# Kernel tuning notes

Measured on AMD Instinct MI355X. Metric: run time of the kernel, lower is better.

## Reference

```python
import jax, jax.numpy as jnp
import numpy as np

H = 16           # num_heads
D = 1024         # hidden_size
HD = D // H      # head_dim = 64
LN_EPS = 1e-5


def setup_inputs() -> dict:
    key = jax.random.key(0)
    ks = jax.random.split(key, 11)
    s = 1.0 / np.sqrt(D)
    x = jax.random.normal(ks[0], (2, 2048, D), dtype=jnp.float32)
    Wq = jax.random.uniform(ks[1], (D, D), jnp.float32, -s, s)
    bq = jax.random.uniform(ks[2], (D,), jnp.float32, -s, s)
    Wk = jax.random.uniform(ks[3], (D, D), jnp.float32, -s, s)
    bk = jax.random.uniform(ks[4], (D,), jnp.float32, -s, s)
    Wv = jax.random.uniform(ks[5], (D, D), jnp.float32, -s, s)
    bv = jax.random.uniform(ks[6], (D,), jnp.float32, -s, s)
    Wo = jax.random.uniform(ks[7], (D, D), jnp.float32, -s, s)
    bo = jax.random.uniform(ks[8], (D,), jnp.float32, -s, s)
    gamma = jnp.ones((D,), jnp.float32)
    beta = jnp.zeros((D,), jnp.float32)
    return {"x": x, "Wq": Wq, "bq": bq, "Wk": Wk, "bk": bk,
            "Wv": Wv, "bv": bv, "Wo": Wo, "bo": bo,
            "gamma": gamma, "beta": beta}


def reference(x, Wq, bq, Wk, bk, Wv, bv, Wo, bo, gamma, beta):
    B, S, _ = x.shape
    # projections -> [B, H, S, HD]
    def split_heads(t):
        return t.reshape(B, S, H, HD).transpose(0, 2, 1, 3)
    Q = split_heads(x @ Wq + bq)
    K = split_heads(x @ Wk + bk)
    V = split_heads(x @ Wv + bv)
    # scores [B, H, S, S], softmax over keys (dropout = identity in eval)
    scores = jnp.einsum('bhqd,bhkd->bhqk', Q, K) / np.sqrt(HD).astype(np.float32)
    attn = jax.nn.softmax(scores, axis=-1)
    ctx = jnp.einsum('bhqk,bhkd->bhqd', attn, V)          # [B, H, S, HD]
    ctx = ctx.transpose(0, 2, 1, 3).reshape(B, S, H * HD)  # [B, S, D]
    out = ctx @ Wo + bo
    # residual + LayerNorm
    y = out + x
    mu = jnp.mean(y, axis=-1, keepdims=True)
    var = jnp.mean(jnp.square(y - mu), axis=-1, keepdims=True)
    return (y - mu) * jax.lax.rsqrt(var + LN_EPS) * gamma + beta
```

## Files before the change

### kernel.cpp

```cpp
#include <hip/hip_runtime.h>
#include <cstdint>
#include <cstddef>


typedef short  b16x8  __attribute__((ext_vector_type(8)));
typedef float  f32x4  __attribute__((ext_vector_type(4)));
typedef float  f32x16 __attribute__((ext_vector_type(16)));

#define AS1 __attribute__((address_space(1)))
#define AS3 __attribute__((address_space(3)))

__device__ __forceinline__ unsigned short f2bf(float f) {
    unsigned int u = __builtin_bit_cast(unsigned int, f);
    u += 0x7FFFu + ((u >> 16) & 1u);
    return (unsigned short)(u >> 16);
}

__device__ __forceinline__ unsigned int cvt_pk_bf16(float lo, float hi) {
    unsigned int r;
    asm("v_cvt_pk_bf16_f32 %0, %1, %2" : "=v"(r) : "v"(lo), "v"(hi));
    return r;
}

__device__ __forceinline__ float exp2_fast(float x) {
    float r;
    asm("v_exp_f32 %0, %1" : "=v"(r) : "v"(x));
    return r;
}

__device__ __forceinline__ void permswap(unsigned &a, unsigned &b) {
    asm volatile("v_permlane32_swap_b32 %0, %1" : "+v"(a), "+v"(b));
}

__global__ __launch_bounds__(256) void k_cvt_x(const float* __restrict__ x,
                                               unsigned short* __restrict__ xb) {
    int i = blockIdx.x * 256 + threadIdx.x;
    float4 v = ((const float4*)x)[i];
    ushort4 o;
    o.x = f2bf(v.x); o.y = f2bf(v.y); o.z = f2bf(v.z); o.w = f2bf(v.w);
    ((ushort4*)xb)[i] = o;
}

__global__ __launch_bounds__(1024) void k_cvt_w(
    const float* __restrict__ W0, const float* __restrict__ W1,
    const float* __restrict__ W2, const float* __restrict__ W3,
    unsigned short* __restrict__ T0, unsigned short* __restrict__ T1,
    unsigned short* __restrict__ T2, unsigned short* __restrict__ T3) {
    const float* W = blockIdx.z == 0 ? W0 : blockIdx.z == 1 ? W1 : blockIdx.z == 2 ? W2 : W3;
    unsigned short* T = blockIdx.z == 0 ? T0 : blockIdx.z == 1 ? T1 : blockIdx.z == 2 ? T2 : T3;
    __shared__ float tile[32][33];
    int k0 = blockIdx.x * 32, n0 = blockIdx.y * 32;
    int tx = threadIdx.x, ty = threadIdx.y;
    tile[ty][tx] = W[(size_t)(k0 + ty) * 1024 + n0 + tx];
    __syncthreads();
    T[(size_t)(n0 + ty) * 1024 + k0 + tx] = f2bf(tile[tx][ty]);
}

__global__ __launch_bounds__(512) void k_gemm_qkv(
    const unsigned short* __restrict__ A, const unsigned short* __restrict__ Bt,
    const float* __restrict__ bq, const float* __restrict__ bk, const float* __restrict__ bv,
    unsigned short* __restrict__ Qb, unsigned short* __restrict__ Kt,
    unsigned short* __restrict__ Vt) {
    __shared__ unsigned short As[2][256 * 32];
    __shared__ unsigned short Bs[2][96 * 32];
    const int tid = threadIdx.x, lane = tid & 63, wid = tid >> 6;
    const int m0 = blockIdx.y * 256, n0 = blockIdx.x * 96;
    const int wr = wid >> 1, wc = wid & 1;
    f32x4 acc[4][3] = {};

    const int srow = tid >> 2, scol = (tid & 3) * 8;
    const unsigned short* Ag  = A  + (size_t)(m0 + srow) * 1024 + scol;
    const unsigned short* Ag2 = A  + (size_t)(m0 + 128 + srow) * 1024 + scol;
    const unsigned short* Bg  = Bt + (size_t)(n0 + srow) * 1024 + scol;

#define GSTAGE(kt, buf) do {                                                              \
        __builtin_amdgcn_global_load_lds((const AS1 void*)(Ag  + (kt) * 32),              \
                                         (AS3 void*)((char*)As[buf] + tid * 16),        16, 0, 0); \
        __builtin_amdgcn_global_load_lds((const AS1 void*)(Ag2 + (kt) * 32),              \
                                         (AS3 void*)((char*)As[buf] + 8192 + tid * 16), 16, 0, 0); \
        if (tid < 384)                                                                    \
            __builtin_amdgcn_global_load_lds((const AS1 void*)(Bg + (kt) * 32),           \
                                             (AS3 void*)((char*)Bs[buf] + tid * 16),    16, 0, 0); \
    } while (0)

    GSTAGE(0, 0);
    __syncthreads();

    const int g = lane >> 4, r = lane & 15;
    for (int kt = 0; kt < 32; ++kt) {
        const int cur = kt & 1;
        if (kt < 31) GSTAGE(kt + 1, cur ^ 1);
        b16x8 af[4], bfr[3];
#pragma unroll
        for (int mi = 0; mi < 4; ++mi)
            af[mi] = __builtin_bit_cast(b16x8, *(const uint4*)(As[cur] + (wr * 64 + mi * 16 + r) * 32 + g * 8));
#pragma unroll
        for (int ni = 0; ni < 3; ++ni)
            bfr[ni] = __builtin_bit_cast(b16x8, *(const uint4*)(Bs[cur] + (wc * 48 + ni * 16 + r) * 32 + g * 8));
#pragma unroll
        for (int mi = 0; mi < 4; ++mi)
#pragma unroll
            for (int ni = 0; ni < 3; ++ni)
                acc[mi][ni] = __builtin_amdgcn_mfma_f32_16x16x32_bf16(af[mi], bfr[ni], acc[mi][ni], 0, 0, 0);
        __syncthreads();
    }
#undef GSTAGE

    for (int ni = 0; ni < 3; ++ni) {
        int col = n0 + wc * 48 + ni * 16 + r;
        int which = col >> 10, c = col & 1023;
        const float* bp = which == 0 ? bq : which == 1 ? bk : bv;
        float bvv = bp[c];
        int h = c >> 6, hd = c & 63;
        for (int mi = 0; mi < 4; ++mi)
            for (int j = 0; j < 4; ++j) {
                int row = m0 + wr * 64 + mi * 16 + g * 4 + j;
                float v = acc[mi][ni][j] + bvv;
                int b = row >> 11, s = row & 2047;
                size_t bh = (size_t)(b * 16 + h);
                if (which == 0) {
                    Qb[(bh * 2048 + s) * 64 + hd] = f2bf(v * 0.180336881f);
                } else if (which == 1) {
                    int tt = s >> 6, kr = s & 63;
                    Kt[(bh * 32 + tt) * 4096 + ((kr * 64 + hd) ^ ((kr & 7) << 3))] = f2bf(v);
                } else {
                    int tt = s >> 6, cc = s & 63;
                    Vt[(bh * 32 + tt) * 4096 + ((hd * 64 + cc) ^ ((hd & 7) << 3))] = f2bf(v);
                }
            }
    }
}

__global__ __launch_bounds__(512) void k_gemm_proj(
    const unsigned short* __restrict__ A, const unsigned short* __restrict__ Bt,
    const float* __restrict__ bias, float* __restrict__ out) {
    __shared__ unsigned short As[2][128 * 32];
    __shared__ unsigned short Bs[2][64 * 32];
    const int tid = threadIdx.x, lane = tid & 63, wid = tid >> 6;
    const int m0 = blockIdx.y * 128, n0 = blockIdx.x * 64;
    const int wr = wid >> 1, wc = wid & 1;
    f32x4 acc[2][2] = {};

    const int srow = tid >> 2, scol = (tid & 3) * 8;
    const unsigned short* Ag = A  + (size_t)(m0 + srow) * 1024 + scol;
    const unsigned short* Bg = Bt + (size_t)(n0 + srow) * 1024 + scol;

#define PSTAGE(kt, buf) do {                                                              \
        __builtin_amdgcn_global_load_lds((const AS1 void*)(Ag + (kt) * 32),               \
                                         (AS3 void*)((char*)As[buf] + tid * 16), 16, 0, 0); \
        if (tid < 256)                                                                    \
            __builtin_amdgcn_global_load_lds((const AS1 void*)(Bg + (kt) * 32),           \
                                             (AS3 void*)((char*)Bs[buf] + tid * 16), 16, 0, 0); \
    } while (0)

    PSTAGE(0, 0);
    __syncthreads();

    const int g = lane >> 4, r = lane & 15;
    for (int kt = 0; kt < 32; ++kt) {
        const int cur = kt & 1;
        if (kt < 31) PSTAGE(kt + 1, cur ^ 1);
        b16x8 af[2], bfr[2];
#pragma unroll
        for (int mi = 0; mi < 2; ++mi)
            af[mi] = __builtin_bit_cast(b16x8, *(const uint4*)(As[cur] + (wr * 32 + mi * 16 + r) * 32 + g * 8));
#pragma unroll
        for (int ni = 0; ni < 2; ++ni)
            bfr[ni] = __builtin_bit_cast(b16x8, *(const uint4*)(Bs[cur] + (wc * 32 + ni * 16 + r) * 32 + g * 8));
#pragma unroll
        for (int mi = 0; mi < 2; ++mi)
#pragma unroll
            for (int ni = 0; ni < 2; ++ni)
                acc[mi][ni] = __builtin_amdgcn_mfma_f32_16x16x32_bf16(af[mi], bfr[ni], acc[mi][ni], 0, 0, 0);
        __syncthreads();
    }
#undef PSTAGE

    for (int mi = 0; mi < 2; ++mi)
        for (int ni = 0; ni < 2; ++ni) {
            int col = n0 + wc * 32 + ni * 16 + r;
            float bv = bias[col];
            for (int j = 0; j < 4; ++j) {
                int row = m0 + wr * 32 + mi * 16 + g * 4 + j;
                out[(size_t)row * 1024 + col] = acc[mi][ni][j] + bv;
            }
        }
}

#define TSWZ(row, byteoff) ((((row) * 128) + (byteoff)) ^ (((row) & 7) << 4))

__global__ __launch_bounds__(256, 2) void k_attn(const unsigned short* __restrict__ Qb,
                                                 const unsigned short* __restrict__ Kt,
                                                 const unsigned short* __restrict__ Vt,
                                                 unsigned short* __restrict__ ctx) {
    __shared__ unsigned short Ks[2][4096];
    __shared__ unsigned short Vs[2][4096];
    const int tid = threadIdx.x, lane = tid & 63, w = tid >> 6;
    const int q32 = lane & 31, hi = lane >> 5;

    int bid = blockIdx.x;
    int xcd = bid & 7, idx = bid >> 3;
    int bh = xcd * 4 + (idx & 3);
    int q0 = (idx >> 2) * 128;
    const int b = bh >> 4, h = bh & 15;

    const unsigned short* qrow = Qb + ((size_t)bh * 2048 + q0 + w * 32 + q32) * 64 + hi * 8;
    b16x8 qf[4];
#pragma unroll
    for (int ds = 0; ds < 4; ++ds)
        qf[ds] = __builtin_bit_cast(b16x8, *(const uint4*)(qrow + ds * 16));

    const unsigned short* Kg = Kt + (size_t)bh * 32 * 4096;
    const unsigned short* Vg = Vt + (size_t)bh * 32 * 4096;

#define STAGE(kt, buf) do {                                                               \
        const unsigned short* _ks = Kg + (size_t)(kt) * 4096 + tid * 8;                   \
        const unsigned short* _vs = Vg + (size_t)(kt) * 4096 + tid * 8;                   \
        __builtin_amdgcn_global_load_lds((const AS1 void*)_ks,          (AS3 void*)((char*)Ks[buf] + tid * 16),        16, 0, 0); \
        __builtin_amdgcn_global_load_lds((const AS1 void*)(_ks + 2048), (AS3 void*)((char*)Ks[buf] + 4096 + tid * 16), 16, 0, 0); \
        __builtin_amdgcn_global_load_lds((const AS1 void*)_vs,          (AS3 void*)((char*)Vs[buf] + tid * 16),        16, 0, 0); \
        __builtin_amdgcn_global_load_lds((const AS1 void*)(_vs + 2048), (AS3 void*)((char*)Vs[buf] + 4096 + tid * 16), 16, 0, 0); \
    } while (0)

    float m_run = -1e30f, lpart = 0.f;
    f32x16 oacc[2] = {};

    STAGE(0, 0);
    __syncthreads();

    for (int kt = 0; kt < 32; ++kt) {
        const int cur = kt & 1;
        if (kt < 31) STAGE(kt + 1, cur ^ 1);

        f32x16 sacc[2] = {};
#pragma unroll
        for (int ds = 0; ds < 4; ++ds) {
            b16x8 kf0 = __builtin_bit_cast(b16x8, *(const uint4*)((char*)Ks[cur] + TSWZ(q32,      ds * 32 + hi * 16)));
            b16x8 kf1 = __builtin_bit_cast(b16x8, *(const uint4*)((char*)Ks[cur] + TSWZ(32 + q32, ds * 32 + hi * 16)));
            sacc[0] = __builtin_amdgcn_mfma_f32_32x32x16_bf16(kf0, qf[ds], sacc[0], 0, 0, 0);
            sacc[1] = __builtin_amdgcn_mfma_f32_32x32x16_bf16(kf1, qf[ds], sacc[1], 0, 0, 0);
        }

        float m8[8];
#pragma unroll
        for (int i = 0; i < 8; ++i)
            m8[i] = fmaxf(fmaxf(sacc[0][i], sacc[0][i + 8]), fmaxf(sacc[1][i], sacc[1][i + 8]));
        float mx = fmaxf(fmaxf(fmaxf(m8[0], m8[1]), fmaxf(m8[2], m8[3])),
                         fmaxf(fmaxf(m8[4], m8[5]), fmaxf(m8[6], m8[7])));
        {
            unsigned a = __builtin_bit_cast(unsigned, mx), bb = a;
            permswap(a, bb);
            mx = fmaxf(__builtin_bit_cast(float, a), __builtin_bit_cast(float, bb));
        }
        if (!__all(mx <= m_run + 8.f)) {
            float mn = fmaxf(m_run, mx);
            float al = exp2_fast(m_run - mn);
            m_run = mn;
            lpart *= al;
#pragma unroll
            for (int reg = 0; reg < 16; ++reg) {
                int qr = (reg & 3) + 8 * (reg >> 2) + 4 * hi;
                float ar = __shfl(al, qr, 64);
                oacc[0][reg] *= ar;
                oacc[1][reg] *= ar;
            }
        }
        float pb[2][16];
#pragma unroll
        for (int kb = 0; kb < 2; ++kb)
#pragma unroll
            for (int reg = 0; reg < 16; ++reg) {
                float p = exp2_fast(sacc[kb][reg] - m_run);
                pb[kb][reg] = p;
                lpart += p;
            }
        unsigned wv[2][4][2];
#pragma unroll
        for (int kb = 0; kb < 2; ++kb)
#pragma unroll
            for (int rg = 0; rg < 4; ++rg) {
                wv[kb][rg][0] = cvt_pk_bf16(pb[kb][rg * 4 + 0], pb[kb][rg * 4 + 1]);
                wv[kb][rg][1] = cvt_pk_bf16(pb[kb][rg * 4 + 2], pb[kb][rg * 4 + 3]);
            }
        b16x8 pa[4];
#pragma unroll
        for (int ks = 0; ks < 4; ++ks) {
            int kb = ks >> 1, rg0 = (ks & 1) * 2;
            unsigned u0 = wv[kb][rg0][0], u2 = wv[kb][rg0 + 1][0];
            permswap(u0, u2);
            unsigned u1 = wv[kb][rg0][1], u3 = wv[kb][rg0 + 1][1];
            permswap(u1, u3);
            uint4 uu; uu.x = u0; uu.y = u1; uu.z = u2; uu.w = u3;
            pa[ks] = __builtin_bit_cast(b16x8, uu);
        }
#pragma unroll
        for (int ks = 0; ks < 4; ++ks) {
            b16x8 vf0 = __builtin_bit_cast(b16x8, *(const uint4*)((char*)Vs[cur] + TSWZ(q32,      ks * 32 + hi * 16)));
            b16x8 vf1 = __builtin_bit_cast(b16x8, *(const uint4*)((char*)Vs[cur] + TSWZ(32 + q32, ks * 32 + hi * 16)));
            oacc[0] = __builtin_amdgcn_mfma_f32_32x32x16_bf16(pa[ks], vf0, oacc[0], 0, 0, 0);
            oacc[1] = __builtin_amdgcn_mfma_f32_32x32x16_bf16(pa[ks], vf1, oacc[1], 0, 0, 0);
        }
        __syncthreads();
    }

    {
        unsigned a = __builtin_bit_cast(unsigned, lpart), bb = a;
        permswap(a, bb);
        lpart = __builtin_bit_cast(float, a) + __builtin_bit_cast(float, bb);
    }
    float invl = 1.f / lpart;
#pragma unroll
    for (int reg = 0; reg < 16; ++reg) {
        int qr = (reg & 3) + 8 * (reg >> 2) + 4 * hi;
        float iv = __shfl(invl, qr, 64);
        unsigned short* dst = ctx + ((size_t)(b * 2048 + q0 + w * 32 + qr)) * 1024 + h * 64 + q32;
        dst[0]  = f2bf(oacc[0][reg] * iv);
        dst[32] = f2bf(oacc[1][reg] * iv);
    }
#undef STAGE
}

__global__ __launch_bounds__(256) void k_ln(const float* __restrict__ proj,
                                            const float* __restrict__ x,
                                            const float* __restrict__ gamma,
                                            const float* __restrict__ beta,
                                            float* __restrict__ out) {
    int t = threadIdx.x, lane = t & 63, w = t >> 6;
    int row = blockIdx.x * 4 + w;
    const float4* pr = (const float4*)(proj + (size_t)row * 1024);
    const float4* xr = (const float4*)(x    + (size_t)row * 1024);
    float4 y[4];
    float s = 0.f, ss = 0.f;
#pragma unroll
    for (int i = 0; i < 4; ++i) {
        float4 a = pr[lane + i * 64], bx = xr[lane + i * 64];
        float4 yy;
        yy.x = a.x + bx.x; yy.y = a.y + bx.y; yy.z = a.z + bx.z; yy.w = a.w + bx.w;
        y[i] = yy;
        s  += yy.x + yy.y + yy.z + yy.w;
        ss += yy.x * yy.x + yy.y * yy.y + yy.z * yy.z + yy.w * yy.w;
    }
#pragma unroll
    for (int o = 32; o > 0; o >>= 1) {
        s  += __shfl_xor(s,  o, 64);
        ss += __shfl_xor(ss, o, 64);
    }
    float mu  = s * (1.f / 1024.f);
    float var = ss * (1.f / 1024.f) - mu * mu;
    float inv = rsqrtf(var + 1e-5f);
    float4* outr = (float4*)(out + (size_t)row * 1024);
    const float4* gr = (const float4*)gamma;
    const float4* br = (const float4*)beta;
#pragma unroll
    for (int i = 0; i < 4; ++i) {
        float4 g4 = gr[lane + i * 64], b4 = br[lane + i * 64];
        float4 o4;
        o4.x = (y[i].x - mu) * inv * g4.x + b4.x;
        o4.y = (y[i].y - mu) * inv * g4.y + b4.y;
        o4.z = (y[i].z - mu) * inv * g4.z + b4.z;
        o4.w = (y[i].w - mu) * inv * g4.w + b4.w;
        outr[lane + i * 64] = o4;
    }
}

extern "C" void kernel_launch(void* const* d_in, const int* in_sizes, int n_in,
                              void* d_out, int out_size, void* d_ws, size_t ws_size,
                              hipStream_t stream) {
    const float* x  = (const float*)d_in[0];
    const float* Wq = (const float*)d_in[1];
    const float* bq = (const float*)d_in[2];
    const float* Wk = (const float*)d_in[3];
    const float* bk = (const float*)d_in[4];
    const float* Wv = (const float*)d_in[5];
    const float* bv = (const float*)d_in[6];
    const float* Wo = (const float*)d_in[7];
    const float* bo = (const float*)d_in[8];
    const float* gamma = (const float*)d_in[9];
    const float* beta  = (const float*)d_in[10];

    char* ws = (char*)d_ws;
    const size_t MB = 1u << 20;
    unsigned short* xbf   = (unsigned short*)(ws);
    unsigned short* Wqkvt = (unsigned short*)(ws + 8 * MB);
    unsigned short* Wot   = (unsigned short*)(ws + 14 * MB);
    unsigned short* Qb    = (unsigned short*)(ws + 16 * MB);
    unsigned short* Kt    = (unsigned short*)(ws + 24 * MB);
    unsigned short* Vt    = (unsigned short*)(ws + 32 * MB);
    float* proj = (float*)(ws + 16 * MB);
    unsigned short* ctx = xbf;

    k_cvt_x<<<4096, 256, 0, stream>>>(x, xbf);
    k_cvt_w<<<dim3(32, 32, 4), dim3(32, 32), 0, stream>>>(
        Wq, Wk, Wv, Wo, Wqkvt, Wqkvt + 1024 * 1024, Wqkvt + 2 * 1024 * 1024, Wot);
    k_gemm_qkv<<<dim3(32, 16), 512, 0, stream>>>(xbf, Wqkvt, bq, bk, bv, Qb, Kt, Vt);
    k_attn<<<512, 256, 0, stream>>>(Qb, Kt, Vt, ctx);
    k_gemm_proj<<<dim3(16, 32), 512, 0, stream>>>(ctx, Wot, bo, proj);
    k_ln<<<1024, 256, 0, stream>>>(proj, x, gamma, beta, (float*)d_out);
}
```

Before: 141.3 us.

## Split attention KV range across two warp groups and merge partial softmax results

The attention kernel now launches 512 threads per block. Two groups of four waves each process half of the 32 key tiles for the same 128 queries, each group with its own double-buffered K/V LDS region. At the end, group 1 writes its partial output accumulators and (max, sum) into reused LDS, and group 0 combines them with a log-sum-exp rescale before writing ctx. This split-K scheme adds parallelism per block to hide latency, at the cost of doubled LDS use, an extra merge step, and lower register budget per thread under the new launch bounds.

```diff
diff --git a/kernel.cpp b/kernel.cpp
--- a/kernel.cpp
+++ b/kernel.cpp
@@ -189,14 +189,17 @@
 
 #define TSWZ(row, byteoff) ((((row) * 128) + (byteoff)) ^ (((row) & 7) << 4))
 
-__global__ __launch_bounds__(256, 2) void k_attn(const unsigned short* __restrict__ Qb,
+__global__ __launch_bounds__(512, 4) void k_attn(const unsigned short* __restrict__ Qb,
                                                  const unsigned short* __restrict__ Kt,
                                                  const unsigned short* __restrict__ Vt,
                                                  unsigned short* __restrict__ ctx) {
-    __shared__ unsigned short Ks[2][4096];
-    __shared__ unsigned short Vs[2][4096];
+    __shared__ unsigned short Ks[2][2][4096];
+    __shared__ unsigned short Vs[2][2][4096];
+    __shared__ float2 ml[4][64];
     const int tid = threadIdx.x, lane = tid & 63, w = tid >> 6;
     const int q32 = lane & 31, hi = lane >> 5;
+    const int wq = w & 3, grp = w >> 2;
+    const int lt = wq * 64 + lane;
 
     int bid = blockIdx.x;
     int xcd = bid & 7, idx = bid >> 3;
@@ -204,7 +207,7 @@
     int q0 = (idx >> 2) * 128;
     const int b = bh >> 4, h = bh & 15;
 
-    const unsigned short* qrow = Qb + ((size_t)bh * 2048 + q0 + w * 32 + q32) * 64 + hi * 8;
+    const unsigned short* qrow = Qb + ((size_t)bh * 2048 + q0 + wq * 32 + q32) * 64 + hi * 8;
     b16x8 qf[4];
 #pragma unroll
     for (int ds = 0; ds < 4; ++ds)
@@ -212,14 +215,15 @@
 
     const unsigned short* Kg = Kt + (size_t)bh * 32 * 4096;
     const unsigned short* Vg = Vt + (size_t)bh * 32 * 4096;
-
-#define STAGE(kt, buf) do {                                                               \
-        const unsigned short* _ks = Kg + (size_t)(kt) * 4096 + tid * 8;                   \
-        const unsigned short* _vs = Vg + (size_t)(kt) * 4096 + tid * 8;                   \
-        __builtin_amdgcn_global_load_lds((const AS1 void*)_ks,          (AS3 void*)((char*)Ks[buf] + tid * 16),        16, 0, 0); \
-        __builtin_amdgcn_global_load_lds((const AS1 void*)(_ks + 2048), (AS3 void*)((char*)Ks[buf] + 4096 + tid * 16), 16, 0, 0); \
-        __builtin_amdgcn_global_load_lds((const AS1 void*)_vs,          (AS3 void*)((char*)Vs[buf] + tid * 16),        16, 0, 0); \
-        __builtin_amdgcn_global_load_lds((const AS1 void*)(_vs + 2048), (AS3 void*)((char*)Vs[buf] + 4096 + tid * 16), 16, 0, 0); \
+    const int ktbase = grp * 16;
+
+#define STAGE(i, buf) do {                                                                \
+        const unsigned short* _ks = Kg + (size_t)(ktbase + (i)) * 4096 + lt * 8;          \
+        const unsigned short* _vs = Vg + (size_t)(ktbase + (i)) * 4096 + lt * 8;          \
+        __builtin_amdgcn_global_load_lds((const AS1 void*)_ks,          (AS3 void*)((char*)Ks[grp][buf] + lt * 16),        16, 0, 0); \
+        __builtin_amdgcn_global_load_lds((const AS1 void*)(_ks + 2048), (AS3 void*)((char*)Ks[grp][buf] + 4096 + lt * 16), 16, 0, 0); \
+        __builtin_amdgcn_global_load_lds((const AS1 void*)_vs,          (AS3 void*)((char*)Vs[grp][buf] + lt * 16),        16, 0, 0); \
+        __builtin_amdgcn_global_load_lds((const AS1 void*)(_vs + 2048), (AS3 void*)((char*)Vs[grp][buf] + 4096 + lt * 16), 16, 0, 0); \
     } while (0)
 
     float m_run = -1e30f, lpart = 0.f;
@@ -228,23 +232,23 @@
     STAGE(0, 0);
     __syncthreads();
 
-    for (int kt = 0; kt < 32; ++kt) {
-        const int cur = kt & 1;
-        if (kt < 31) STAGE(kt + 1, cur ^ 1);
+    for (int i = 0; i < 16; ++i) {
+        const int cur = i & 1;
+        if (i < 15) STAGE(i + 1, cur ^ 1);
 
         f32x16 sacc[2] = {};
 #pragma unroll
         for (int ds = 0; ds < 4; ++ds) {
-            b16x8 kf0 = __builtin_bit_cast(b16x8, *(const uint4*)((char*)Ks[cur] + TSWZ(q32,      ds * 32 + hi * 16)));
-            b16x8 kf1 = __builtin_bit_cast(b16x8, *(const uint4*)((char*)Ks[cur] + TSWZ(32 + q32, ds * 32 + hi * 16)));
+            b16x8 kf0 = __builtin_bit_cast(b16x8, *(const uint4*)((char*)Ks[grp][cur] + TSWZ(q32,      ds * 32 + hi * 16)));
+            b16x8 kf1 = __builtin_bit_cast(b16x8, *(const uint4*)((char*)Ks[grp][cur] + TSWZ(32 + q32, ds * 32 + hi * 16)));
             sacc[0] = __builtin_amdgcn_mfma_f32_32x32x16_bf16(kf0, qf[ds], sacc[0], 0, 0, 0);
             sacc[1] = __builtin_amdgcn_mfma_f32_32x32x16_bf16(kf1, qf[ds], sacc[1], 0, 0, 0);
         }
 
         float m8[8];
 #pragma unroll
-        for (int i = 0; i < 8; ++i)
-            m8[i] = fmaxf(fmaxf(sacc[0][i], sacc[0][i + 8]), fmaxf(sacc[1][i], sacc[1][i + 8]));
+        for (int i2 = 0; i2 < 8; ++i2)
+            m8[i2] = fmaxf(fmaxf(sacc[0][i2], sacc[0][i2 + 8]), fmaxf(sacc[1][i2], sacc[1][i2 + 8]));
         float mx = fmaxf(fmaxf(fmaxf(m8[0], m8[1]), fmaxf(m8[2], m8[3])),
                          fmaxf(fmaxf(m8[4], m8[5]), fmaxf(m8[6], m8[7])));
         {
@@ -295,8 +299,8 @@
         }
 #pragma unroll
         for (int ks = 0; ks < 4; ++ks) {
-            b16x8 vf0 = __builtin_bit_cast(b16x8, *(const uint4*)((char*)Vs[cur] + TSWZ(q32,      ks * 32 + hi * 16)));
-            b16x8 vf1 = __builtin_bit_cast(b16x8, *(const uint4*)((char*)Vs[cur] + TSWZ(32 + q32, ks * 32 + hi * 16)));
+            b16x8 vf0 = __builtin_bit_cast(b16x8, *(const uint4*)((char*)Vs[grp][cur] + TSWZ(q32,      ks * 32 + hi * 16)));
+            b16x8 vf1 = __builtin_bit_cast(b16x8, *(const uint4*)((char*)Vs[grp][cur] + TSWZ(32 + q32, ks * 32 + hi * 16)));
             oacc[0] = __builtin_amdgcn_mfma_f32_32x32x16_bf16(pa[ks], vf0, oacc[0], 0, 0, 0);
             oacc[1] = __builtin_amdgcn_mfma_f32_32x32x16_bf16(pa[ks], vf1, oacc[1], 0, 0, 0);
         }
@@ -308,14 +312,38 @@
         permswap(a, bb);
         lpart = __builtin_bit_cast(float, a) + __builtin_bit_cast(float, bb);
     }
-    float invl = 1.f / lpart;
-#pragma unroll
-    for (int reg = 0; reg < 16; ++reg) {
-        int qr = (reg & 3) + 8 * (reg >> 2) + 4 * hi;
-        float iv = __shfl(invl, qr, 64);
-        unsigned short* dst = ctx + ((size_t)(b * 2048 + q0 + w * 32 + qr)) * 1024 + h * 64 + q32;
-        dst[0]  = f2bf(oacc[0][reg] * iv);
-        dst[32] = f2bf(oacc[1][reg] * iv);
+
+    float* s0 = (float*)Ks[1];
+    float* s1 = (float*)Vs[1];
+    if (grp == 1) {
+        int base = (wq * 64 + lane) * 16;
+#pragma unroll
+        for (int reg = 0; reg < 16; ++reg) {
+            s0[base + reg] = oacc[0][reg];
+            s1[base + reg] = oacc[1][reg];
+        }
+        ml[wq][lane] = make_float2(m_run, lpart);
+    }
+    __syncthreads();
+    if (grp == 0) {
+        float2 p1 = ml[wq][lane];
+        float m  = fmaxf(m_run, p1.x);
+        float a0 = exp2_fast(m_run - m), a1 = exp2_fast(p1.x - m);
+        float l  = lpart * a0 + p1.y * a1;
+        float inv = 1.f / l;
+        float f0 = a0 * inv, f1 = a1 * inv;
+        int base = (wq * 64 + lane) * 16;
+#pragma unroll
+        for (int reg = 0; reg < 16; ++reg) {
+            int qr = (reg & 3) + 8 * (reg >> 2) + 4 * hi;
+            float g0 = __shfl(f0, qr, 64);
+            float g1 = __shfl(f1, qr, 64);
+            float o0 = oacc[0][reg] * g0 + s0[base + reg] * g1;
+            float o1 = oacc[1][reg] * g0 + s1[base + reg] * g1;
+            unsigned short* dst = ctx + ((size_t)(b * 2048 + q0 + wq * 32 + qr)) * 1024 + h * 64 + q32;
+            dst[0]  = f2bf(o0);
+            dst[32] = f2bf(o1);
+        }
     }
 #undef STAGE
 }
@@ -393,7 +421,7 @@
     k_cvt_w<<<dim3(32, 32, 4), dim3(32, 32), 0, stream>>>(
         Wq, Wk, Wv, Wo, Wqkvt, Wqkvt + 1024 * 1024, Wqkvt + 2 * 1024 * 1024, Wot);
     k_gemm_qkv<<<dim3(32, 16), 512, 0, stream>>>(xbf, Wqkvt, bq, bk, bv, Qb, Kt, Vt);
-    k_attn<<<512, 256, 0, stream>>>(Qb, Kt, Vt, ctx);
+    k_attn<<<512, 512, 0, stream>>>(Qb, Kt, Vt, ctx);
     k_gemm_proj<<<dim3(16, 32), 512, 0, stream>>>(ctx, Wot, bo, proj);
     k_ln<<<1024, 256, 0, stream>>>(proj, x, gamma, beta, (float*)d_out);
 }
```

Result: faster. 138.4 us (-2.1%).
